# Kernel tuning notes

Measured on AMD Instinct MI355X. Metric: run time of the kernel, lower is better.

Reference implementation:

```python
import jax, jax.numpy as jnp
import numpy as np

NUM_HEADS = 16
LN_EPS = 1e-5


def setup_inputs() -> dict:
    key = jax.random.key(0)
    ks = jax.random.split(key, 6)
    b, s, d = 2, 2048, 1024
    scale = 1.0 / np.sqrt(d)
    return {
        "x": jax.random.normal(ks[0], (b, s, d), dtype=jnp.float32),
        "W_w": jax.random.normal(ks[1], (3 * d, d), dtype=jnp.float32) * scale,
        "W_b": jax.random.normal(ks[2], (3 * d,), dtype=jnp.float32) * 0.01,
        "proj_w": jax.random.normal(ks[3], (d, d), dtype=jnp.float32) * scale,
        "proj_b": jax.random.normal(ks[4], (d,), dtype=jnp.float32) * 0.01,
        "gamma": jnp.ones((d,), dtype=jnp.float32),
        "beta": jnp.zeros((d,), dtype=jnp.float32),
    }


def reference(x, W_w, W_b, proj_w, proj_b, gamma, beta):
    b, s, d = x.shape
    h = NUM_HEADS
    hd = d // h
    # fused QKV projection: [b,s,3d]
    qkv = x @ W_w.T + W_b
    q, k, v = jnp.split(qkv, 3, axis=-1)
    # [b,s,d] -> [b,h,s,hd]
    q, k, v = (z.reshape(b, s, h, hd).transpose(0, 2, 1, 3) for z in (q, k, v))
    # NOTE: original scales by sqrt(d), not sqrt(head_dim)
    attn = jnp.einsum('bhqd,bhkd->bhqk', q, k) / jnp.sqrt(jnp.asarray(d, x.dtype))
    attn_weights = jax.nn.softmax(attn, axis=-1)  # [b,h,s,s]
    o = jnp.einsum('bhqk,bhkd->bhqd', attn_weights, v)
    o = o.transpose(0, 2, 1, 3).reshape(b, s, d)
    out = o @ proj_w.T + proj_b  # dropout is identity at eval
    y = x + out
    mu = jnp.mean(y, axis=-1, keepdims=True)
    var = jnp.var(y, axis=-1, keepdims=True)
    y_norm = (y - mu) / jnp.sqrt(var + LN_EPS) * gamma + beta
    return (y_norm, attn_weights)
```

## Files before the change

kernel.cpp:

```cpp
#include <hip/hip_runtime.h>
#include <cstdint>

#define BB 2
#define SS 2048
#define DD 1024
#define HH 16
#define HDIM 64
#define MM (BB*SS)
#define N3 (3*DD)

typedef __attribute__((ext_vector_type(4))) float f32x4;
typedef __attribute__((ext_vector_type(8))) __bf16 bf16x8;

static __device__ __forceinline__ unsigned short f2bf_fast(float f) {
  __bf16 h = (__bf16)f;
  return __builtin_bit_cast(unsigned short, h);
}

static __device__ __forceinline__ uint4 pack8f(const float4 a, const float4 b) {
  union { unsigned short us[8]; uint4 v; } pk;
  pk.us[0] = f2bf_fast(a.x); pk.us[1] = f2bf_fast(a.y); pk.us[2] = f2bf_fast(a.z); pk.us[3] = f2bf_fast(a.w);
  pk.us[4] = f2bf_fast(b.x); pk.us[5] = f2bf_fast(b.y); pk.us[6] = f2bf_fast(b.z); pk.us[7] = f2bf_fast(b.w);
  return pk.v;
}

static __device__ __forceinline__ void gload16(const unsigned short* g, unsigned short* l) {
  __builtin_amdgcn_global_load_lds(
      (const __attribute__((address_space(1))) void*)g,
      (__attribute__((address_space(3))) void*)l, 16, 0, 0);
}

__global__ __launch_bounds__(256) void cvt_kernel(
    const float* __restrict__ x, const float* __restrict__ Ww,
    const float* __restrict__ pw,
    unsigned short* __restrict__ xb, unsigned short* __restrict__ Wwb,
    unsigned short* __restrict__ pwb) {
  const size_t i = ((size_t)blockIdx.x * 256 + threadIdx.x) * 8;
  const float* src;
  unsigned short* dst;
  if (i < 4194304u)       { src = x  + i;            dst = xb  + i; }
  else if (i < 7340032u)  { src = Ww + (i - 4194304u); dst = Wwb + (i - 4194304u); }
  else                    { src = pw + (i - 7340032u); dst = pwb + (i - 7340032u); }
  const float4* s4 = (const float4*)src;
  *(uint4*)dst = pack8f(s4[0], s4[1]);
}

__global__ __launch_bounds__(256) void gemm_qkv(
    const unsigned short* __restrict__ xb, const unsigned short* __restrict__ Wwb,
    const float* __restrict__ Wb,
    unsigned short* __restrict__ qb, unsigned short* __restrict__ kb,
    unsigned short* __restrict__ vbT) {
  __shared__ __align__(16) unsigned short As[128 * 32];
  __shared__ __align__(16) unsigned short Bs[128 * 32];
  const int t = threadIdx.x;
  const int l = t & 63, w = t >> 6;
  const int wr = w >> 1, wc = w & 1;
  const int m0 = blockIdx.y * 128, n0 = blockIdx.x * 128;
  f32x4 acc[4][4] = {};

  for (int kt = 0; kt < DD; kt += 32) {
    __syncthreads();
    #pragma unroll
    for (int i = 0; i < 2; ++i) {
      const int row = (i * 4 + w) * 16 + (l >> 2);
      const int cc = (l & 3) * 8;
      gload16(xb  + (size_t)(m0 + row) * DD + kt + cc, &As[(i * 4 + w) * 512]);
      gload16(Wwb + (size_t)(n0 + row) * DD + kt + cc, &Bs[(i * 4 + w) * 512]);
    }
    __syncthreads();
    bf16x8 a[4], b[4];
    #pragma unroll
    for (int i = 0; i < 4; ++i) {
      a[i] = __builtin_bit_cast(bf16x8, *(const uint4*)&As[(wr * 64 + i * 16 + (l & 15)) * 32 + (l >> 4) * 8]);
      b[i] = __builtin_bit_cast(bf16x8, *(const uint4*)&Bs[(wc * 64 + i * 16 + (l & 15)) * 32 + (l >> 4) * 8]);
    }
    #pragma unroll
    for (int i = 0; i < 4; ++i)
      #pragma unroll
      for (int j = 0; j < 4; ++j)
        acc[i][j] = __builtin_amdgcn_mfma_f32_16x16x32_bf16(a[i], b[j], acc[i][j], 0, 0, 0);
  }

  #pragma unroll
  for (int i = 0; i < 4; ++i)
    #pragma unroll
    for (int j = 0; j < 4; ++j)
      #pragma unroll
      for (int r = 0; r < 4; ++r) {
        const int row = m0 + wr * 64 + i * 16 + (l >> 4) * 4 + r;
        const int col = n0 + wc * 64 + j * 16 + (l & 15);
        const float v = acc[i][j][r] + Wb[col];
        const int bidx = row >> 11;
        const int srow = row & 2047;
        const int which = col >> 10;
        const int cc = col & 1023;
        const int head = cc >> 6;
        const int hd = cc & 63;
        if (which == 0) {
          qb[((size_t)((bidx * HH + head) * SS + srow)) * HDIM + hd] = f2bf_fast(v * 0.04508422f);
        } else if (which == 1) {
          kb[((size_t)((bidx * HH + head) * SS + srow)) * HDIM + hd] = f2bf_fast(v);
        } else {
          vbT[((size_t)(bidx * HH + head) * HDIM + hd) * SS + srow] = f2bf_fast(v);
        }
      }
}

__global__ __launch_bounds__(256) void attn_kernel(
    const unsigned short* __restrict__ qb,
    const unsigned short* __restrict__ kb,
    const unsigned short* __restrict__ vbT,
    unsigned short* __restrict__ ob,
    float* __restrict__ attn_out) {
  __shared__ float Ored[4][64][68];
  __shared__ float Lred[4][64];
  const int t = threadIdx.x;
  const int l = t & 63, w = t >> 6;
  const int q_l = l & 15, hi = l >> 4;
  const int bid = blockIdx.x;
  const int swz = (bid & 7) * 128 + (bid >> 3);
  const int bh = swz >> 5;
  const int q0 = (swz & 31) * 64;
  const size_t base = (size_t)bh * SS * HDIM;

  bf16x8 qa[4][2];
  #pragma unroll
  for (int j = 0; j < 4; ++j)
    #pragma unroll
    for (int kc = 0; kc < 2; ++kc)
      qa[j][kc] = __builtin_bit_cast(bf16x8,
          *(const uint4*)(qb + base + (size_t)(q0 + j * 16 + q_l) * HDIM + kc * 32 + hi * 8));

  const unsigned short* kga = kb + base + (size_t)(w * 16 + q_l) * HDIM + hi * 8;
  const unsigned short* vga = vbT + ((size_t)bh * HDIM + q_l) * SS + w * 16 + hi * 4;

  float lsum[4] = {0.f, 0.f, 0.f, 0.f};
  {
    uint4 k0 = *(const uint4*)(kga);
    uint4 k1 = *(const uint4*)(kga + 32);
    for (int kt = 0; kt < SS; kt += 64) {
      const bool more = (kt + 64) < SS;
      uint4 n0, n1;
      if (more) {
        n0 = *(const uint4*)(kga + (size_t)(kt + 64) * HDIM);
        n1 = *(const uint4*)(kga + (size_t)(kt + 64) * HDIM + 32);
      }
      f32x4 sQ[4] = {};
      const bf16x8 kf0 = __builtin_bit_cast(bf16x8, k0);
      const bf16x8 kf1 = __builtin_bit_cast(bf16x8, k1);
      __builtin_amdgcn_s_setprio(1);
      #pragma unroll
      for (int j = 0; j < 4; ++j) {
        sQ[j] = __builtin_amdgcn_mfma_f32_16x16x32_bf16(kf0, qa[j][0], sQ[j], 0, 0, 0);
        sQ[j] = __builtin_amdgcn_mfma_f32_16x16x32_bf16(kf1, qa[j][1], sQ[j], 0, 0, 0);
      }
      __builtin_amdgcn_s_setprio(0);
      #pragma unroll
      for (int j = 0; j < 4; ++j)
        #pragma unroll
        for (int r = 0; r < 4; ++r)
          lsum[j] += __builtin_amdgcn_exp2f(sQ[j][r]);
      k0 = n0; k1 = n1;
    }
  }
  #pragma unroll
  for (int j = 0; j < 4; ++j) {
    float s = lsum[j];
    s += __shfl_xor(s, 16);
    s += __shfl_xor(s, 32);
    lsum[j] = s;
  }
  if (hi == 0) {
    #pragma unroll
    for (int j = 0; j < 4; ++j) Lred[w][j * 16 + q_l] = lsum[j];
  }
  __syncthreads();
  float rl[4];
  #pragma unroll
  for (int j = 0; j < 4; ++j)
    rl[j] = 1.0f / (Lred[0][j * 16 + q_l] + Lred[1][j * 16 + q_l] +
                    Lred[2][j * 16 + q_l] + Lred[3][j * 16 + q_l]);

  float* pbs[4];
  #pragma unroll
  for (int j = 0; j < 4; ++j)
    pbs[j] = attn_out + ((size_t)bh * SS + (q0 + j * 16 + q_l)) * SS + w * 16 + hi * 4;

  f32x4 of[4][4] = {};
  {
    uint4 k0 = *(const uint4*)(kga);
    uint4 k1 = *(const uint4*)(kga + 32);
    uint2 vv[4];
    #pragma unroll
    for (int d4 = 0; d4 < 4; ++d4)
      vv[d4] = *(const uint2*)(vga + (size_t)(d4 * 16) * SS);
    for (int kt = 0; kt < SS; kt += 64) {
      const bool more = (kt + 64) < SS;
      uint4 n0, n1; uint2 nv[4];
      if (more) {
        n0 = *(const uint4*)(kga + (size_t)(kt + 64) * HDIM);
        n1 = *(const uint4*)(kga + (size_t)(kt + 64) * HDIM + 32);
        #pragma unroll
        for (int d4 = 0; d4 < 4; ++d4)
          nv[d4] = *(const uint2*)(vga + (size_t)(d4 * 16) * SS + kt + 64);
      }
      f32x4 sQ[4] = {};
      const bf16x8 kf0 = __builtin_bit_cast(bf16x8, k0);
      const bf16x8 kf1 = __builtin_bit_cast(bf16x8, k1);
      __builtin_amdgcn_s_setprio(1);
      #pragma unroll
      for (int j = 0; j < 4; ++j) {
        sQ[j] = __builtin_amdgcn_mfma_f32_16x16x32_bf16(kf0, qa[j][0], sQ[j], 0, 0, 0);
        sQ[j] = __builtin_amdgcn_mfma_f32_16x16x32_bf16(kf1, qa[j][1], sQ[j], 0, 0, 0);
      }
      __builtin_amdgcn_s_setprio(0);
      bf16x8 pbp[4];
      #pragma unroll
      for (int j = 0; j < 4; ++j) {
        float4 pv;
        pv.x = __builtin_amdgcn_exp2f(sQ[j][0]) * rl[j];
        pv.y = __builtin_amdgcn_exp2f(sQ[j][1]) * rl[j];
        pv.z = __builtin_amdgcn_exp2f(sQ[j][2]) * rl[j];
        pv.w = __builtin_amdgcn_exp2f(sQ[j][3]) * rl[j];
        __builtin_nontemporal_store(*(const f32x4*)&pv, (f32x4*)(pbs[j] + kt));
        union { unsigned short us[8]; uint4 v; } pk;
        pk.us[0] = f2bf_fast(pv.x); pk.us[1] = f2bf_fast(pv.y);
        pk.us[2] = f2bf_fast(pv.z); pk.us[3] = f2bf_fast(pv.w);
        pk.us[4] = 0; pk.us[5] = 0; pk.us[6] = 0; pk.us[7] = 0;
        pbp[j] = __builtin_bit_cast(bf16x8, pk.v);
      }
      __builtin_amdgcn_s_setprio(1);
      #pragma unroll
      for (int d4 = 0; d4 < 4; ++d4) {
        uint4 vp; vp.x = vv[d4].x; vp.y = vv[d4].y; vp.z = 0u; vp.w = 0u;
        const bf16x8 vfp = __builtin_bit_cast(bf16x8, vp);
        #pragma unroll
        for (int j = 0; j < 4; ++j)
          of[d4][j] = __builtin_amdgcn_mfma_f32_16x16x32_bf16(vfp, pbp[j], of[d4][j], 0, 0, 0);
      }
      __builtin_amdgcn_s_setprio(0);
      k0 = n0; k1 = n1;
      #pragma unroll
      for (int d4 = 0; d4 < 4; ++d4) vv[d4] = nv[d4];
    }
  }

  #pragma unroll
  for (int d4 = 0; d4 < 4; ++d4)
    #pragma unroll
    for (int j = 0; j < 4; ++j)
      *(f32x4*)&Ored[w][j * 16 + q_l][d4 * 16 + hi * 4] = of[d4][j];
  __syncthreads();
  const int bidx = bh >> 4, h_ = bh & 15;
  const int qf = w * 16 + q_l;
  union { unsigned short us[16]; uint4 v[2]; } opk;
  #pragma unroll
  for (int c4 = 0; c4 < 4; ++c4) {
    const int d0 = hi * 16 + c4 * 4;
    f32x4 s = *(const f32x4*)&Ored[0][qf][d0];
    s += *(const f32x4*)&Ored[1][qf][d0];
    s += *(const f32x4*)&Ored[2][qf][d0];
    s += *(const f32x4*)&Ored[3][qf][d0];
    opk.us[c4 * 4 + 0] = f2bf_fast(s[0]);
    opk.us[c4 * 4 + 1] = f2bf_fast(s[1]);
    opk.us[c4 * 4 + 2] = f2bf_fast(s[2]);
    opk.us[c4 * 4 + 3] = f2bf_fast(s[3]);
  }
  unsigned short* orow = ob + ((size_t)bidx * SS + (q0 + qf)) * DD + h_ * 64 + hi * 16;
  *(uint4*)orow = opk.v[0];
  *(uint4*)(orow + 8) = opk.v[1];
}

__global__ __launch_bounds__(256) void gemm_proj(
    const unsigned short* __restrict__ ob, const unsigned short* __restrict__ pwb,
    const float* __restrict__ pb, const float* __restrict__ x,
    float* __restrict__ y) {
  __shared__ __align__(16) unsigned short As[128 * 32];
  __shared__ __align__(16) unsigned short Bs[128 * 32];
  const int t = threadIdx.x;
  const int l = t & 63, w = t >> 6;
  const int wr = w >> 1, wc = w & 1;
  const int m0 = blockIdx.y * 128, n0 = blockIdx.x * 128;
  f32x4 acc[4][4] = {};

  for (int kt = 0; kt < DD; kt += 32) {
    __syncthreads();
    #pragma unroll
    for (int i = 0; i < 2; ++i) {
      const int row = (i * 4 + w) * 16 + (l >> 2);
      const int cc = (l & 3) * 8;
      gload16(ob  + (size_t)(m0 + row) * DD + kt + cc, &As[(i * 4 + w) * 512]);
      gload16(pwb + (size_t)(n0 + row) * DD + kt + cc, &Bs[(i * 4 + w) * 512]);
    }
    __syncthreads();
    bf16x8 a[4], b[4];
    #pragma unroll
    for (int i = 0; i < 4; ++i) {
      a[i] = __builtin_bit_cast(bf16x8, *(const uint4*)&As[(wr * 64 + i * 16 + (l & 15)) * 32 + (l >> 4) * 8]);
      b[i] = __builtin_bit_cast(bf16x8, *(const uint4*)&Bs[(wc * 64 + i * 16 + (l & 15)) * 32 + (l >> 4) * 8]);
    }
    #pragma unroll
    for (int i = 0; i < 4; ++i)
      #pragma unroll
      for (int j = 0; j < 4; ++j)
        acc[i][j] = __builtin_amdgcn_mfma_f32_16x16x32_bf16(a[i], b[j], acc[i][j], 0, 0, 0);
  }
  #pragma unroll
  for (int i = 0; i < 4; ++i)
    #pragma unroll
    for (int j = 0; j < 4; ++j)
      #pragma unroll
      for (int r = 0; r < 4; ++r) {
        const int row = m0 + wr * 64 + i * 16 + (l >> 4) * 4 + r;
        const int col = n0 + wc * 64 + j * 16 + (l & 15);
        const size_t idx = (size_t)row * DD + col;
        y[idx] = acc[i][j][r] + pb[col] + x[idx];
      }
}

__global__ __launch_bounds__(256) void ln_kernel(
    float* __restrict__ y, const float* __restrict__ gamma,
    const float* __restrict__ beta) {
  const int row = blockIdx.x;
  const int t = threadIdx.x;
  const float4 v = ((const float4*)(y + (size_t)row * DD))[t];
  float s  = v.x + v.y + v.z + v.w;
  float s2 = v.x * v.x + v.y * v.y + v.z * v.z + v.w * v.w;
  #pragma unroll
  for (int off = 1; off < 64; off <<= 1) { s += __shfl_xor(s, off); s2 += __shfl_xor(s2, off); }
  __shared__ float red[8];
  const int l = t & 63, w = t >> 6;
  if (l == 0) { red[w] = s; red[4 + w] = s2; }
  __syncthreads();
  s  = red[0] + red[1] + red[2] + red[3];
  s2 = red[4] + red[5] + red[6] + red[7];
  const float mu = s * (1.0f / DD);
  const float var = s2 * (1.0f / DD) - mu * mu;
  const float rs = rsqrtf(var + 1e-5f);
  const float4 g  = ((const float4*)gamma)[t];
  const float4 be = ((const float4*)beta)[t];
  float4 o;
  o.x = (v.x - mu) * rs * g.x + be.x;
  o.y = (v.y - mu) * rs * g.y + be.y;
  o.z = (v.z - mu) * rs * g.z + be.z;
  o.w = (v.w - mu) * rs * g.w + be.w;
  ((float4*)(y + (size_t)row * DD))[t] = o;
}

extern "C" void kernel_launch(void* const* d_in, const int* in_sizes, int n_in,
                              void* d_out, int out_size, void* d_ws, size_t ws_size,
                              hipStream_t stream) {
  const float* x     = (const float*)d_in[0];
  const float* Ww    = (const float*)d_in[1];
  const float* Wb    = (const float*)d_in[2];
  const float* Pw    = (const float*)d_in[3];
  const float* Pb    = (const float*)d_in[4];
  const float* gamma = (const float*)d_in[5];
  const float* beta  = (const float*)d_in[6];

  float* out      = (float*)d_out;
  float* y_norm   = out;
  float* attn_out = out + (size_t)MM * DD;

  char* ws = (char*)d_ws;
  unsigned short* qb  = (unsigned short*)(ws);
  unsigned short* kb  = (unsigned short*)(ws +  8388608);
  unsigned short* vbT = (unsigned short*)(ws + 16777216);
  unsigned short* ob  = (unsigned short*)(ws + 25165824);
  unsigned short* xb  = (unsigned short*)(ws + 33554432);
  unsigned short* Wwb = (unsigned short*)(ws + 41943040);
  unsigned short* pwb = (unsigned short*)(ws + 48234496);

  cvt_kernel<<<4096, 256, 0, stream>>>(x, Ww, Pw, xb, Wwb, pwb);
  gemm_qkv<<<dim3(N3 / 128, MM / 128), 256, 0, stream>>>(xb, Wwb, Wb, qb, kb, vbT);
  attn_kernel<<<1024, 256, 0, stream>>>(qb, kb, vbT, ob, attn_out);
  gemm_proj<<<dim3(DD / 128, MM / 128), 256, 0, stream>>>(ob, pwb, Pb, x, y_norm);
  ln_kernel<<<MM, 256, 0, stream>>>(y_norm, gamma, beta);
}
```

Baseline: 262.6 us.

## Halve attention query tile to double blocks; stage V transpose through shared memory

The attention kernel now handles 32 queries per block instead of 64 and launches 2048 blocks. This halves per-block register and accumulator state and gives more parallelism. The cost is that each K/V tile is streamed from global memory twice as often overall. V prefetching is dropped in favour of loading V at the top of each iteration. Separately, the QKV GEMM epilogue writes V blocks through a padded shared-memory transpose so the transposed V output uses 16-byte coalesced stores instead of scattered 2-byte ones.

Result: slower. 352.4 us (+34.2%).

```diff
diff --git a/kernel.cpp b/kernel.cpp
--- a/kernel.cpp
+++ b/kernel.cpp
@@ -50,8 +50,9 @@
     const float* __restrict__ Wb,
     unsigned short* __restrict__ qb, unsigned short* __restrict__ kb,
     unsigned short* __restrict__ vbT) {
-  __shared__ __align__(16) unsigned short As[128 * 32];
-  __shared__ __align__(16) unsigned short Bs[128 * 32];
+  __shared__ __align__(16) unsigned short Sh[128 * 132];
+  unsigned short* As = Sh;
+  unsigned short* Bs = Sh + 128 * 32;
   const int t = threadIdx.x;
   const int l = t & 63, w = t >> 6;
   const int wr = w >> 1, wc = w & 1;
@@ -80,30 +81,56 @@
       for (int j = 0; j < 4; ++j)
         acc[i][j] = __builtin_amdgcn_mfma_f32_16x16x32_bf16(a[i], b[j], acc[i][j], 0, 0, 0);
   }
-
-  #pragma unroll
-  for (int i = 0; i < 4; ++i)
-    #pragma unroll
-    for (int j = 0; j < 4; ++j)
-      #pragma unroll
-      for (int r = 0; r < 4; ++r) {
-        const int row = m0 + wr * 64 + i * 16 + (l >> 4) * 4 + r;
-        const int col = n0 + wc * 64 + j * 16 + (l & 15);
-        const float v = acc[i][j][r] + Wb[col];
-        const int bidx = row >> 11;
-        const int srow = row & 2047;
-        const int which = col >> 10;
-        const int cc = col & 1023;
-        const int head = cc >> 6;
-        const int hd = cc & 63;
-        if (which == 0) {
-          qb[((size_t)((bidx * HH + head) * SS + srow)) * HDIM + hd] = f2bf_fast(v * 0.04508422f);
-        } else if (which == 1) {
-          kb[((size_t)((bidx * HH + head) * SS + srow)) * HDIM + hd] = f2bf_fast(v);
-        } else {
-          vbT[((size_t)(bidx * HH + head) * HDIM + hd) * SS + srow] = f2bf_fast(v);
+  __syncthreads();
+
+  if (n0 < 2048) {
+    const bool isq = (n0 < 1024);
+    #pragma unroll
+    for (int i = 0; i < 4; ++i)
+      #pragma unroll
+      for (int j = 0; j < 4; ++j)
+        #pragma unroll
+        for (int r = 0; r < 4; ++r) {
+          const int row = m0 + wr * 64 + i * 16 + (l >> 4) * 4 + r;
+          const int col = n0 + wc * 64 + j * 16 + (l & 15);
+          const float v = acc[i][j][r] + Wb[col];
+          const int bidx = row >> 11, srow = row & 2047;
+          const int cc = col & 1023, head = cc >> 6, hd = cc & 63;
+          const size_t idx = ((size_t)((bidx * HH + head) * SS + srow)) * HDIM + hd;
+          if (isq) qb[idx] = f2bf_fast(v * 0.04508422f);
+          else     kb[idx] = f2bf_fast(v);
         }
-      }
+  } else {
+    unsigned short* Tt = Sh;
+    #pragma unroll
+    for (int i = 0; i < 4; ++i)
+      #pragma unroll
+      for (int j = 0; j < 4; ++j)
+        #pragma unroll
+        for (int r = 0; r < 4; ++r) {
+          const int rr = wr * 64 + i * 16 + (l >> 4) * 4 + r;
+          const int cl = wc * 64 + j * 16 + (l & 15);
+          Tt[rr * 132 + cl] = f2bf_fast(acc[i][j][r] + Wb[n0 + cl]);
+        }
+    __syncthreads();
+    const int bidx = m0 >> 11, srow0 = m0 & 2047;
+    const int q = t & 3;
+    #pragma unroll
+    for (int ci = 0; ci < 2; ++ci) {
+      const int c = ci * 64 + (t >> 2);
+      const int vcol = n0 - 2048 + c;
+      const int head = vcol >> 6, hd = vcol & 63;
+      unsigned short* dst = vbT + ((size_t)(bidx * HH + head) * HDIM + hd) * SS + srow0;
+      #pragma unroll
+      for (int e8 = 0; e8 < 4; ++e8) {
+        const int r0 = e8 * 32 + q * 8;
+        union { unsigned short us[8]; uint4 v; } pk;
+        #pragma unroll
+        for (int e = 0; e < 8; ++e) pk.us[e] = Tt[(r0 + e) * 132 + c];
+        *(uint4*)(dst + r0) = pk.v;
+      }
+    }
+  }
 }
 
 __global__ __launch_bounds__(256) void attn_kernel(
@@ -112,20 +139,20 @@
     const unsigned short* __restrict__ vbT,
     unsigned short* __restrict__ ob,
     float* __restrict__ attn_out) {
-  __shared__ float Ored[4][64][68];
-  __shared__ float Lred[4][64];
+  __shared__ float Ored[4][32][68];
+  __shared__ float Lred[4][32];
   const int t = threadIdx.x;
   const int l = t & 63, w = t >> 6;
   const int q_l = l & 15, hi = l >> 4;
   const int bid = blockIdx.x;
-  const int swz = (bid & 7) * 128 + (bid >> 3);
-  const int bh = swz >> 5;
-  const int q0 = (swz & 31) * 64;
+  const int swz = (bid & 7) * 256 + (bid >> 3);
+  const int bh = swz >> 6;
+  const int q0 = (swz & 63) * 32;
   const size_t base = (size_t)bh * SS * HDIM;
 
-  bf16x8 qa[4][2];
-  #pragma unroll
-  for (int j = 0; j < 4; ++j)
+  bf16x8 qa[2][2];
+  #pragma unroll
+  for (int j = 0; j < 2; ++j)
     #pragma unroll
     for (int kc = 0; kc < 2; ++kc)
       qa[j][kc] = __builtin_bit_cast(bf16x8,
@@ -134,37 +161,37 @@
   const unsigned short* kga = kb + base + (size_t)(w * 16 + q_l) * HDIM + hi * 8;
   const unsigned short* vga = vbT + ((size_t)bh * HDIM + q_l) * SS + w * 16 + hi * 4;
 
-  float lsum[4] = {0.f, 0.f, 0.f, 0.f};
+  float lsum[2] = {0.f, 0.f};
   {
     uint4 k0 = *(const uint4*)(kga);
     uint4 k1 = *(const uint4*)(kga + 32);
     for (int kt = 0; kt < SS; kt += 64) {
       const bool more = (kt + 64) < SS;
-      uint4 n0, n1;
+      uint4 p0, p1;
       if (more) {
-        n0 = *(const uint4*)(kga + (size_t)(kt + 64) * HDIM);
-        n1 = *(const uint4*)(kga + (size_t)(kt + 64) * HDIM + 32);
-      }
-      f32x4 sQ[4] = {};
+        p0 = *(const uint4*)(kga + (size_t)(kt + 64) * HDIM);
+        p1 = *(const uint4*)(kga + (size_t)(kt + 64) * HDIM + 32);
+      }
+      f32x4 sQ[2] = {};
       const bf16x8 kf0 = __builtin_bit_cast(bf16x8, k0);
       const bf16x8 kf1 = __builtin_bit_cast(bf16x8, k1);
       __builtin_amdgcn_s_setprio(1);
       #pragma unroll
-      for (int j = 0; j < 4; ++j) {
+      for (int j = 0; j < 2; ++j) {
         sQ[j] = __builtin_amdgcn_mfma_f32_16x16x32_bf16(kf0, qa[j][0], sQ[j], 0, 0, 0);
         sQ[j] = __builtin_amdgcn_mfma_f32_16x16x32_bf16(kf1, qa[j][1], sQ[j], 0, 0, 0);
       }
       __builtin_amdgcn_s_setprio(0);
       #pragma unroll
-      for (int j = 0; j < 4; ++j)
+      for (int j = 0; j < 2; ++j)
         #pragma unroll
         for (int r = 0; r < 4; ++r)
           lsum[j] += __builtin_amdgcn_exp2f(sQ[j][r]);
-      k0 = n0; k1 = n1;
-    }
-  }
-  #pragma unroll
-  for (int j = 0; j < 4; ++j) {
+      if (more) { k0 = p0; k1 = p1; }
+    }
+  }
+  #pragma unroll
+  for (int j = 0; j < 2; ++j) {
     float s = lsum[j];
     s += __shfl_xor(s, 16);
     s += __shfl_xor(s, 32);
@@ -172,51 +199,48 @@
   }
   if (hi == 0) {
     #pragma unroll
-    for (int j = 0; j < 4; ++j) Lred[w][j * 16 + q_l] = lsum[j];
+    for (int j = 0; j < 2; ++j) Lred[w][j * 16 + q_l] = lsum[j];
   }
   __syncthreads();
-  float rl[4];
-  #pragma unroll
-  for (int j = 0; j < 4; ++j)
+  float rl[2];
+  #pragma unroll
+  for (int j = 0; j < 2; ++j)
     rl[j] = 1.0f / (Lred[0][j * 16 + q_l] + Lred[1][j * 16 + q_l] +
                     Lred[2][j * 16 + q_l] + Lred[3][j * 16 + q_l]);
 
-  float* pbs[4];
-  #pragma unroll
-  for (int j = 0; j < 4; ++j)
+  float* pbs[2];
+  #pragma unroll
+  for (int j = 0; j < 2; ++j)
     pbs[j] = attn_out + ((size_t)bh * SS + (q0 + j * 16 + q_l)) * SS + w * 16 + hi * 4;
 
-  f32x4 of[4][4] = {};
+  f32x4 of[4][2] = {};
   {
     uint4 k0 = *(const uint4*)(kga);
     uint4 k1 = *(const uint4*)(kga + 32);
-    uint2 vv[4];
-    #pragma unroll
-    for (int d4 = 0; d4 < 4; ++d4)
-      vv[d4] = *(const uint2*)(vga + (size_t)(d4 * 16) * SS);
     for (int kt = 0; kt < SS; kt += 64) {
       const bool more = (kt + 64) < SS;
-      uint4 n0, n1; uint2 nv[4];
+      uint2 vv[4];
+      #pragma unroll
+      for (int d4 = 0; d4 < 4; ++d4)
+        vv[d4] = *(const uint2*)(vga + (size_t)(d4 * 16) * SS + kt);
+      uint4 p0, p1;
       if (more) {
-        n0 = *(const uint4*)(kga + (size_t)(kt + 64) * HDIM);
-        n1 = *(const uint4*)(kga + (size_t)(kt + 64) * HDIM + 32);
-        #pragma unroll
-        for (int d4 = 0; d4 < 4; ++d4)
-          nv[d4] = *(const uint2*)(vga + (size_t)(d4 * 16) * SS + kt + 64);
-      }
-      f32x4 sQ[4] = {};
+        p0 = *(const uint4*)(kga + (size_t)(kt + 64) * HDIM);
+        p1 = *(const uint4*)(kga + (size_t)(kt + 64) * HDIM + 32);
+      }
+      f32x4 sQ[2] = {};
       const bf16x8 kf0 = __builtin_bit_cast(bf16x8, k0);
       const bf16x8 kf1 = __builtin_bit_cast(bf16x8, k1);
       __builtin_amdgcn_s_setprio(1);
       #pragma unroll
-      for (int j = 0; j < 4; ++j) {
+      for (int j = 0; j < 2; ++j) {
         sQ[j] = __builtin_amdgcn_mfma_f32_16x16x32_bf16(kf0, qa[j][0], sQ[j], 0, 0, 0);
         sQ[j] = __builtin_amdgcn_mfma_f32_16x16x32_bf16(kf1, qa[j][1], sQ[j], 0, 0, 0);
       }
       __builtin_amdgcn_s_setprio(0);
-      bf16x8 pbp[4];
-      #pragma unroll
-      for (int j = 0; j < 4; ++j) {
+      bf16x8 pbp[2];
+      #pragma unroll
+      for (int j = 0; j < 2; ++j) {
         float4 pv;
         pv.x = __builtin_amdgcn_exp2f(sQ[j][0]) * rl[j];
         pv.y = __builtin_amdgcn_exp2f(sQ[j][1]) * rl[j];
@@ -235,40 +259,31 @@
         uint4 vp; vp.x = vv[d4].x; vp.y = vv[d4].y; vp.z = 0u; vp.w = 0u;
         const bf16x8 vfp = __builtin_bit_cast(bf16x8, vp);
         #pragma unroll
-        for (int j = 0; j < 4; ++j)
+        for (int j = 0; j < 2; ++j)
           of[d4][j] = __builtin_amdgcn_mfma_f32_16x16x32_bf16(vfp, pbp[j], of[d4][j], 0, 0, 0);
       }
       __builtin_amdgcn_s_setprio(0);
-      k0 = n0; k1 = n1;
-      #pragma unroll
-      for (int d4 = 0; d4 < 4; ++d4) vv[d4] = nv[d4];
+      if (more) { k0 = p0; k1 = p1; }
     }
   }
 
   #pragma unroll
   for (int d4 = 0; d4 < 4; ++d4)
     #pragma unroll
-    for (int j = 0; j < 4; ++j)
+    for (int j = 0; j < 2; ++j)
       *(f32x4*)&Ored[w][j * 16 + q_l][d4 * 16 + hi * 4] = of[d4][j];
   __syncthreads();
   const int bidx = bh >> 4, h_ = bh & 15;
-  const int qf = w * 16 + q_l;
-  union { unsigned short us[16]; uint4 v[2]; } opk;
-  #pragma unroll
-  for (int c4 = 0; c4 < 4; ++c4) {
-    const int d0 = hi * 16 + c4 * 4;
-    f32x4 s = *(const f32x4*)&Ored[0][qf][d0];
-    s += *(const f32x4*)&Ored[1][qf][d0];
-    s += *(const f32x4*)&Ored[2][qf][d0];
-    s += *(const f32x4*)&Ored[3][qf][d0];
-    opk.us[c4 * 4 + 0] = f2bf_fast(s[0]);
-    opk.us[c4 * 4 + 1] = f2bf_fast(s[1]);
-    opk.us[c4 * 4 + 2] = f2bf_fast(s[2]);
-    opk.us[c4 * 4 + 3] = f2bf_fast(s[3]);
-  }
-  unsigned short* orow = ob + ((size_t)bidx * SS + (q0 + qf)) * DD + h_ * 64 + hi * 16;
-  *(uint4*)orow = opk.v[0];
-  *(uint4*)(orow + 8) = opk.v[1];
+  const int row = t >> 3, seg = t & 7;
+  const int d0 = seg * 8;
+  union { unsigned short us[8]; uint4 v; } opk;
+  #pragma unroll
+  for (int e = 0; e < 8; ++e) {
+    const float s = Ored[0][row][d0 + e] + Ored[1][row][d0 + e] +
+                    Ored[2][row][d0 + e] + Ored[3][row][d0 + e];
+    opk.us[e] = f2bf_fast(s);
+  }
+  *(uint4*)(ob + ((size_t)bidx * SS + (q0 + row)) * DD + h_ * 64 + d0) = opk.v;
 }
 
 __global__ __launch_bounds__(256) void gemm_proj(
@@ -373,7 +388,7 @@
 
   cvt_kernel<<<4096, 256, 0, stream>>>(x, Ww, Pw, xb, Wwb, pwb);
   gemm_qkv<<<dim3(N3 / 128, MM / 128), 256, 0, stream>>>(xb, Wwb, Wb, qb, kb, vbT);
-  attn_kernel<<<1024, 256, 0, stream>>>(qb, kb, vbT, ob, attn_out);
+  attn_kernel<<<2048, 256, 0, stream>>>(qb, kb, vbT, ob, attn_out);
   gemm_proj<<<dim3(DD / 128, MM / 128), 256, 0, stream>>>(ob, pwb, Pb, x, y_norm);
   ln_kernel<<<MM, 256, 0, stream>>>(y_norm, gamma, beta);
 }
```
